# Performance work log

Hardware: AMD Instinct MI355X
Metric: run time of the kernel (lower is better)

Reference implementation:

```python
import jax, jax.numpy as jnp
import numpy as np

N_KERNELS = 5
MUL_FACTOR = 2.0


def setup_inputs() -> dict:
    key = jax.random.key(0)
    k1, k2 = jax.random.split(key)
    X = jax.random.normal(k1, (4096, 512), dtype=jnp.float32)
    Y = jax.random.normal(k2, (4096, 512), dtype=jnp.float32)
    return {"X": X, "Y": Y}


def _mmd(X, Y):
    # multipliers: 2.0 ** (arange(5) - 2) = [0.25, 0.5, 1, 2, 4]
    mults = MUL_FACTOR ** (jnp.arange(N_KERNELS, dtype=jnp.float32) - N_KERNELS // 2)
    Z = jnp.concatenate([X, Y], axis=0)            # [N+M, D]
    n = Z.shape[0]
    # squared euclidean pairwise distances (cdist ** 2)
    sq = jnp.sum(Z * Z, axis=-1)                    # [N+M]
    D2 = sq[:, None] + sq[None, :] - 2.0 * (Z @ Z.T)
    D2 = jnp.maximum(D2, 0.0)                       # [N+M, N+M]
    # bandwidth from detached distances: sum / (n^2 - n)
    bw = jax.lax.stop_gradient(jnp.sum(D2)) / (n * n - n)
    # multi-bandwidth RBF sum over kernels
    K = jnp.sum(jnp.exp(-D2[None, :, :] / (bw * mults)[:, None, None]), axis=0)
    Nx = X.shape[0]
    XX = jnp.mean(K[:Nx, :Nx])
    XY = jnp.mean(K[:Nx, Nx:])
    YY = jnp.mean(K[Nx:, Nx:])
    return XX - 2.0 * XY + YY


def reference(X, Y):
    return _mmd(X, Y)
```

## Files before the change

### kernel.cpp

```cpp
#include <hip/hip_runtime.h>

#define N_ROWS 8192
#define NX     4096
#define DIM    512
#define BT     128
#define NT     64
#define BK     32

typedef __bf16 bf16_t;
typedef bf16_t bf16x8 __attribute__((ext_vector_type(8)));
typedef bf16_t bf16x4 __attribute__((ext_vector_type(4)));
typedef float  f32x4  __attribute__((ext_vector_type(4)));

#if __has_builtin(__builtin_amdgcn_exp2f)
  #define EXP2F __builtin_amdgcn_exp2f
#else
  #define EXP2F exp2f
#endif


__device__ __forceinline__ const float* zrow(const float* X, const float* Y, int r) {
    return (r < NX) ? (X + (size_t)r * DIM) : (Y + (size_t)(r - NX) * DIM);
}

__device__ __forceinline__ void gload_lds16(const bf16_t* g, bf16_t* l) {
    __builtin_amdgcn_global_load_lds(
        (__attribute__((address_space(1))) void*)(void*)(g),
        (__attribute__((address_space(3))) void*)(void*)(l), 16, 0, 0);
}

__global__ void k_prep(const float* __restrict__ X, const float* __restrict__ Y,
                       bf16_t* __restrict__ Zh, float* __restrict__ sqrow,
                       float* __restrict__ colsum) {
    int t = threadIdx.x;
    if (blockIdx.x == 0) { colsum[t] = 0.f; colsum[t + 256] = 0.f; }
    int wv = t >> 6, lane = t & 63;
    int row = blockIdx.x * 4 + wv;
    const float4* z4 = (const float4*)zrow(X, Y, row);
    float4 a = z4[lane], b = z4[lane + 64];
    bf16x4 ha = {(bf16_t)a.x, (bf16_t)a.y, (bf16_t)a.z, (bf16_t)a.w};
    bf16x4 hb = {(bf16_t)b.x, (bf16_t)b.y, (bf16_t)b.z, (bf16_t)b.w};
    *(bf16x4*)(Zh + (size_t)row * DIM + lane * 4) = ha;
    *(bf16x4*)(Zh + (size_t)row * DIM + 256 + lane * 4) = hb;
    float s = a.x*a.x + a.y*a.y + a.z*a.z + a.w*a.w
            + b.x*b.x + b.y*b.y + b.z*b.z + b.w*b.w;
    #pragma unroll
    for (int off = 32; off > 0; off >>= 1) s += __shfl_down(s, off);
    if (lane == 0) sqrow[row] = s;
}

__global__ void k_colsum(const float* X, const float* Y, float* colsum) {
    int c = threadIdx.x * 2;
    int r0 = blockIdx.x * 128;
    float s0 = 0.f, s1 = 0.f;
    for (int r = r0; r < r0 + 128; ++r) {
        const float* zr = zrow(X, Y, r);
        float2 v = *(const float2*)(zr + c);
        s0 += v.x; s1 += v.y;
    }
    atomicAdd(&colsum[c], s0);
    atomicAdd(&colsum[c + 1], s1);
}

__global__ void k_bw(const float* sqrow, const float* colsum, float* cvals, double* acc) {
    __shared__ double red[256];
    int t = threadIdx.x;
    double s1 = 0.0;
    for (int i = t; i < N_ROWS; i += 256) s1 += (double)sqrow[i];
    double cs = 0.0;
    for (int d = t; d < DIM; d += 256) { double v = colsum[d]; cs += v * v; }
    red[t] = s1; __syncthreads();
    for (int off = 128; off > 0; off >>= 1) { if (t < off) red[t] += red[t + off]; __syncthreads(); }
    double S1 = red[0]; __syncthreads();
    red[t] = cs; __syncthreads();
    for (int off = 128; off > 0; off >>= 1) { if (t < off) red[t] += red[t + off]; __syncthreads(); }
    if (t == 0) {
        double CS = red[0];
        double n = (double)N_ROWS;
        double sumD2 = 2.0 * n * S1 - 2.0 * CS;
        double bw = sumD2 / (n * n - n);
        const double LOG2E = 1.4426950408889634;
        double mult = 0.25;
        for (int k = 0; k < 5; ++k) {
            cvals[k] = (float)(-LOG2E / (bw * mult));
            mult *= 2.0;
        }
        *acc = 0.0;
    }
}

__global__ __launch_bounds__(256) void k_pair(const bf16_t* __restrict__ Zh,
                                              const float* __restrict__ sqrow,
                                              const float* __restrict__ cvals,
                                              double* acc) {
    int ti = blockIdx.x, tj = blockIdx.y;
    if (tj < ti) return;
    __shared__ bf16_t As[4096];
    __shared__ bf16_t Bs[4096];
    __shared__ float wsum[4];

    int t = threadIdx.x, lane = t & 63, wv = t >> 6;
    int wr = wv >> 1, wc = wv & 1;

    const bf16_t* gA[2]; const bf16_t* gB[2];
    bf16_t* ldsA[2]; bf16_t* ldsB[2];
    #pragma unroll
    for (int h = 0; h < 2; ++h) {
        int c = h * 256 + t;
        int r = c >> 2, sq = c & 3;
        int q = sq ^ ((r >> 1) & 3);
        gA[h] = Zh + (size_t)(ti * BT + r) * DIM + q * 8;
        gB[h] = Zh + (size_t)(tj * BT + r) * DIM + q * 8;
        int base = (h * 256 + wv * 64) * 8;
        ldsA[h] = As + base;
        ldsB[h] = Bs + base;
    }

    int n16 = lane & 15, q16 = lane >> 4;
    int aoff[4], boff[4];
    #pragma unroll
    for (int aa = 0; aa < 4; ++aa) {
        int r = 16 * (wr * 4 + aa) + n16;
        aoff[aa] = (r * 4 + (q16 ^ ((r >> 1) & 3))) * 8;
    }
    #pragma unroll
    for (int bb = 0; bb < 4; ++bb) {
        int r = 16 * (wc * 4 + bb) + n16;
        boff[bb] = (r * 4 + (q16 ^ ((r >> 1) & 3))) * 8;
    }

    f32x4 accf[4][4];
    #pragma unroll
    for (int a = 0; a < 4; ++a)
        #pragma unroll
        for (int b = 0; b < 4; ++b)
            accf[a][b] = (f32x4){0.f, 0.f, 0.f, 0.f};

    for (int kt = 0; kt < DIM; kt += BK) {
        if (kt) __syncthreads();
        #pragma unroll
        for (int h = 0; h < 2; ++h) {
            gload_lds16(gA[h] + kt, ldsA[h]);
            gload_lds16(gB[h] + kt, ldsB[h]);
        }
        __syncthreads();
        bf16x8 a[4], b[4];
        #pragma unroll
        for (int aa = 0; aa < 4; ++aa) a[aa] = *(const bf16x8*)(As + aoff[aa]);
        #pragma unroll
        for (int bb = 0; bb < 4; ++bb) b[bb] = *(const bf16x8*)(Bs + boff[bb]);
        #pragma unroll
        for (int aa = 0; aa < 4; ++aa)
            #pragma unroll
            for (int bb = 0; bb < 4; ++bb)
                accf[aa][bb] = __builtin_amdgcn_mfma_f32_16x16x32_bf16(
                    a[aa], b[bb], accf[aa][bb], 0, 0, 0);
    }

    float c4 = cvals[4];
    int i0 = ti * BT + wr * 64;
    int j0 = tj * BT + wc * 64;

    float sqi[4][4], sqj[4];
    #pragma unroll
    for (int aa = 0; aa < 4; ++aa)
        #pragma unroll
        for (int r = 0; r < 4; ++r)
            sqi[aa][r] = sqrow[i0 + 16 * aa + q16 * 4 + r];
    #pragma unroll
    for (int bb = 0; bb < 4; ++bb)
        sqj[bb] = sqrow[j0 + 16 * bb + n16];

    float s_local = 0.f;
    #pragma unroll
    for (int aa = 0; aa < 4; ++aa) {
        #pragma unroll
        for (int bb = 0; bb < 4; ++bb) {
            #pragma unroll
            for (int r = 0; r < 4; ++r) {
                float d2 = fmaf(-2.f, accf[aa][bb][r], sqi[aa][r] + sqj[bb]);
                d2 = fmaxf(d2, 0.f);
                float e4 = EXP2F(d2 * c4);
                float e3 = e4 * e4;
                float e2 = e3 * e3;
                float e1 = e2 * e2;
                float e0 = e1 * e1;
                s_local += e4 + e3 + e2 + e1 + e0;
            }
        }
    }
    #pragma unroll
    for (int off = 32; off > 0; off >>= 1) s_local += __shfl_down(s_local, off);
    if (lane == 0) wsum[wv] = s_local;
    __syncthreads();
    if (t == 0) {
        float bs = wsum[0] + wsum[1] + wsum[2] + wsum[3];
        double si = (ti < NT / 2) ? 1.0 : -1.0;
        double sj = (tj < NT / 2) ? 1.0 : -1.0;
        double w = si * sj * ((ti == tj) ? 1.0 : 2.0);
        atomicAdd(acc, w * (double)bs);
    }
}

__global__ void k_final(const double* acc, float* out) {
    out[0] = (float)(*acc / ((double)NX * (double)NX));
}

extern "C" void kernel_launch(void* const* d_in, const int* in_sizes, int n_in,
                              void* d_out, int out_size, void* d_ws, size_t ws_size,
                              hipStream_t stream) {
    const float* X = (const float*)d_in[0];
    const float* Y = (const float*)d_in[1];
    float* out = (float*)d_out;

    float*  sqrow  = (float*)d_ws;
    float*  colsum = sqrow + 8192;
    float*  cvals  = (float*)((char*)d_ws + 34816);
    double* acc    = (double*)((char*)d_ws + 34840);
    bf16_t* Zh     = (bf16_t*)((char*)d_ws + 36864);

    k_prep  <<<2048, 256, 0, stream>>>(X, Y, Zh, sqrow, colsum);
    k_colsum<<<64, 256, 0, stream>>>(X, Y, colsum);
    k_bw    <<<1, 256, 0, stream>>>(sqrow, colsum, cvals, acc);
    k_pair  <<<dim3(NT, NT), 256, 0, stream>>>(Zh, sqrow, cvals, acc);
    k_final <<<1, 1, 0, stream>>>(acc, out);
}
```

Measured before the change: 152.8 us.

## Double-buffer pair-kernel LDS tiles, launch only upper-triangle blocks, fuse prep kernels

```diff
diff --git a/kernel.cpp b/kernel.cpp
--- a/kernel.cpp
+++ b/kernel.cpp
@@ -5,7 +5,9 @@
 #define DIM    512
 #define BT     128
 #define NT     64
+#define NB     (NT * (NT + 1) / 2)
 #define BK     32
+#define NCOLB  128
 
 typedef __bf16 bf16_t;
 typedef bf16_t bf16x8 __attribute__((ext_vector_type(8)));
@@ -29,46 +31,52 @@
         (__attribute__((address_space(3))) void*)(void*)(l), 16, 0, 0);
 }
 
-__global__ void k_prep(const float* __restrict__ X, const float* __restrict__ Y,
-                       bf16_t* __restrict__ Zh, float* __restrict__ sqrow,
-                       float* __restrict__ colsum) {
+__global__ void k_prepall(const float* __restrict__ X, const float* __restrict__ Y,
+                          bf16_t* __restrict__ Zh, float* __restrict__ sqrow,
+                          float* __restrict__ colpart) {
     int t = threadIdx.x;
-    if (blockIdx.x == 0) { colsum[t] = 0.f; colsum[t + 256] = 0.f; }
-    int wv = t >> 6, lane = t & 63;
-    int row = blockIdx.x * 4 + wv;
-    const float4* z4 = (const float4*)zrow(X, Y, row);
-    float4 a = z4[lane], b = z4[lane + 64];
-    bf16x4 ha = {(bf16_t)a.x, (bf16_t)a.y, (bf16_t)a.z, (bf16_t)a.w};
-    bf16x4 hb = {(bf16_t)b.x, (bf16_t)b.y, (bf16_t)b.z, (bf16_t)b.w};
-    *(bf16x4*)(Zh + (size_t)row * DIM + lane * 4) = ha;
-    *(bf16x4*)(Zh + (size_t)row * DIM + 256 + lane * 4) = hb;
-    float s = a.x*a.x + a.y*a.y + a.z*a.z + a.w*a.w
-            + b.x*b.x + b.y*b.y + b.z*b.z + b.w*b.w;
-    #pragma unroll
-    for (int off = 32; off > 0; off >>= 1) s += __shfl_down(s, off);
-    if (lane == 0) sqrow[row] = s;
-}
-
-__global__ void k_colsum(const float* X, const float* Y, float* colsum) {
-    int c = threadIdx.x * 2;
-    int r0 = blockIdx.x * 128;
-    float s0 = 0.f, s1 = 0.f;
-    for (int r = r0; r < r0 + 128; ++r) {
-        const float* zr = zrow(X, Y, r);
-        float2 v = *(const float2*)(zr + c);
-        s0 += v.x; s1 += v.y;
-    }
-    atomicAdd(&colsum[c], s0);
-    atomicAdd(&colsum[c + 1], s1);
-}
-
-__global__ void k_bw(const float* sqrow, const float* colsum, float* cvals, double* acc) {
+    if (blockIdx.x < 2048) {
+        int wv = t >> 6, lane = t & 63;
+        int row = blockIdx.x * 4 + wv;
+        const float4* z4 = (const float4*)zrow(X, Y, row);
+        float4 a = z4[lane], b = z4[lane + 64];
+        bf16x4 ha = {(bf16_t)a.x, (bf16_t)a.y, (bf16_t)a.z, (bf16_t)a.w};
+        bf16x4 hb = {(bf16_t)b.x, (bf16_t)b.y, (bf16_t)b.z, (bf16_t)b.w};
+        *(bf16x4*)(Zh + (size_t)row * DIM + lane * 4) = ha;
+        *(bf16x4*)(Zh + (size_t)row * DIM + 256 + lane * 4) = hb;
+        float s = a.x*a.x + a.y*a.y + a.z*a.z + a.w*a.w
+                + b.x*b.x + b.y*b.y + b.z*b.z + b.w*b.w;
+        #pragma unroll
+        for (int off = 32; off > 0; off >>= 1) s += __shfl_down(s, off);
+        if (lane == 0) sqrow[row] = s;
+    } else {
+        int b2 = blockIdx.x - 2048;
+        int c = t * 2;
+        int r0 = b2 * 64;
+        float s0 = 0.f, s1 = 0.f;
+        #pragma unroll 4
+        for (int r = r0; r < r0 + 64; ++r) {
+            float2 v = *(const float2*)(zrow(X, Y, r) + c);
+            s0 += v.x; s1 += v.y;
+        }
+        colpart[b2 * 512 + c]     = s0;
+        colpart[b2 * 512 + c + 1] = s1;
+    }
+}
+
+__global__ void k_bw(const float* __restrict__ sqrow, const float* __restrict__ colpart,
+                     float* cvals, double* acc, unsigned* done) {
     __shared__ double red[256];
     int t = threadIdx.x;
     double s1 = 0.0;
     for (int i = t; i < N_ROWS; i += 256) s1 += (double)sqrow[i];
     double cs = 0.0;
-    for (int d = t; d < DIM; d += 256) { double v = colsum[d]; cs += v * v; }
+    for (int d = t; d < DIM; d += 256) {
+        float tot = 0.f;
+        #pragma unroll 4
+        for (int b = 0; b < NCOLB; ++b) tot += colpart[b * 512 + d];
+        cs += (double)tot * (double)tot;
+    }
     red[t] = s1; __syncthreads();
     for (int off = 128; off > 0; off >>= 1) { if (t < off) red[t] += red[t + off]; __syncthreads(); }
     double S1 = red[0]; __syncthreads();
@@ -86,24 +94,32 @@
             mult *= 2.0;
         }
         *acc = 0.0;
+        *done = 0u;
     }
 }
 
 __global__ __launch_bounds__(256) void k_pair(const bf16_t* __restrict__ Zh,
                                               const float* __restrict__ sqrow,
                                               const float* __restrict__ cvals,
-                                              double* acc) {
-    int ti = blockIdx.x, tj = blockIdx.y;
-    if (tj < ti) return;
-    __shared__ bf16_t As[4096];
-    __shared__ bf16_t Bs[4096];
+                                              double* acc, unsigned* done,
+                                              float* out) {
+    int bid = blockIdx.x;
+    int ti = (int)((2.f * NT + 1.f - sqrtf((float)((2 * NT + 1) * (2 * NT + 1) - 8 * bid))) * 0.5f);
+    #define S_(x) ((x) * NT - (x) * ((x) - 1) / 2)
+    while (S_(ti + 1) <= bid) ++ti;
+    while (S_(ti) > bid) --ti;
+    int tj = ti + (bid - S_(ti));
+    #undef S_
+
+    __shared__ bf16_t As[2][4096];
+    __shared__ bf16_t Bs[2][4096];
     __shared__ float wsum[4];
 
     int t = threadIdx.x, lane = t & 63, wv = t >> 6;
     int wr = wv >> 1, wc = wv & 1;
 
     const bf16_t* gA[2]; const bf16_t* gB[2];
-    bf16_t* ldsA[2]; bf16_t* ldsB[2];
+    int ldsoff[2];
     #pragma unroll
     for (int h = 0; h < 2; ++h) {
         int c = h * 256 + t;
@@ -111,9 +127,7 @@
         int q = sq ^ ((r >> 1) & 3);
         gA[h] = Zh + (size_t)(ti * BT + r) * DIM + q * 8;
         gB[h] = Zh + (size_t)(tj * BT + r) * DIM + q * 8;
-        int base = (h * 256 + wv * 64) * 8;
-        ldsA[h] = As + base;
-        ldsB[h] = Bs + base;
+        ldsoff[h] = (h * 256 + wv * 64) * 8;
     }
 
     int n16 = lane & 15, q16 = lane >> 4;
@@ -136,19 +150,27 @@
         for (int b = 0; b < 4; ++b)
             accf[a][b] = (f32x4){0.f, 0.f, 0.f, 0.f};
 
+    #pragma unroll
+    for (int h = 0; h < 2; ++h) {
+        gload_lds16(gA[h], &As[0][ldsoff[h]]);
+        gload_lds16(gB[h], &Bs[0][ldsoff[h]]);
+    }
+
     for (int kt = 0; kt < DIM; kt += BK) {
-        if (kt) __syncthreads();
-        #pragma unroll
-        for (int h = 0; h < 2; ++h) {
-            gload_lds16(gA[h] + kt, ldsA[h]);
-            gload_lds16(gB[h] + kt, ldsB[h]);
-        }
+        int cur = (kt >> 5) & 1;
         __syncthreads();
+        if (kt + BK < DIM) {
+            #pragma unroll
+            for (int h = 0; h < 2; ++h) {
+                gload_lds16(gA[h] + kt + BK, &As[cur ^ 1][ldsoff[h]]);
+                gload_lds16(gB[h] + kt + BK, &Bs[cur ^ 1][ldsoff[h]]);
+            }
+        }
         bf16x8 a[4], b[4];
         #pragma unroll
-        for (int aa = 0; aa < 4; ++aa) a[aa] = *(const bf16x8*)(As + aoff[aa]);
-        #pragma unroll
-        for (int bb = 0; bb < 4; ++bb) b[bb] = *(const bf16x8*)(Bs + boff[bb]);
+        for (int aa = 0; aa < 4; ++aa) a[aa] = *(const bf16x8*)(&As[cur][aoff[aa]]);
+        #pragma unroll
+        for (int bb = 0; bb < 4; ++bb) b[bb] = *(const bf16x8*)(&Bs[cur][boff[bb]]);
         #pragma unroll
         for (int aa = 0; aa < 4; ++aa)
             #pragma unroll
@@ -199,11 +221,14 @@
         double sj = (tj < NT / 2) ? 1.0 : -1.0;
         double w = si * sj * ((ti == tj) ? 1.0 : 2.0);
         atomicAdd(acc, w * (double)bs);
-    }
-}
-
-__global__ void k_final(const double* acc, float* out) {
-    out[0] = (float)(*acc / ((double)NX * (double)NX));
+        __threadfence();
+        unsigned old = atomicAdd(done, 1u);
+        if (old == NB - 1) {
+            __threadfence();
+            double tot = atomicAdd(acc, 0.0);
+            out[0] = (float)(tot / ((double)NX * (double)NX));
+        }
+    }
 }
 
 extern "C" void kernel_launch(void* const* d_in, const int* in_sizes, int n_in,
@@ -213,15 +238,15 @@
     const float* Y = (const float*)d_in[1];
     float* out = (float*)d_out;
 
-    float*  sqrow  = (float*)d_ws;
-    float*  colsum = sqrow + 8192;
-    float*  cvals  = (float*)((char*)d_ws + 34816);
-    double* acc    = (double*)((char*)d_ws + 34840);
-    bf16_t* Zh     = (bf16_t*)((char*)d_ws + 36864);
-
-    k_prep  <<<2048, 256, 0, stream>>>(X, Y, Zh, sqrow, colsum);
-    k_colsum<<<64, 256, 0, stream>>>(X, Y, colsum);
-    k_bw    <<<1, 256, 0, stream>>>(sqrow, colsum, cvals, acc);
-    k_pair  <<<dim3(NT, NT), 256, 0, stream>>>(Zh, sqrow, cvals, acc);
-    k_final <<<1, 1, 0, stream>>>(acc, out);
-}
+    float*    sqrow   = (float*)d_ws;
+    float*    cvals   = (float*)((char*)d_ws + 32800 - 32);
+    cvals             = (float*)((char*)d_ws + 32768);
+    double*   acc     = (double*)((char*)d_ws + 32800);
+    unsigned* done    = (unsigned*)((char*)d_ws + 32808);
+    float*    colpart = (float*)((char*)d_ws + 32832);
+    bf16_t*   Zh      = (bf16_t*)((char*)d_ws + 294976);
+
+    k_prepall<<<2176, 256, 0, stream>>>(X, Y, Zh, sqrow, colpart);
+    k_bw     <<<1, 256, 0, stream>>>(sqrow, colpart, cvals, acc, done);
+    k_pair   <<<NB, 256, 0, stream>>>(Zh, sqrow, cvals, acc, done, out);
+}
```

Result: slower. 188.4 us (+23.3%).
